# Kernel optimization log

Measured on AMD Instinct MI355X. Metric: run time of the kernel, lower is better.

Reference implementation:

```python
import jax, jax.numpy as jnp
import numpy as np

SOS = 4998
EOS = 4999
SCALING = 2.0


def setup_inputs() -> dict:
    key = jax.random.key(0)
    ks = jax.random.split(key, 12)
    B, T, E, D, A, C, F, ODIM, L = 32, 1000, 512, 1024, 512, 10, 100, 5000, 100
    s = 0.02
    return {
        "hpad": jax.random.normal(ks[0], (B, T, E), jnp.float32),
        "ys": jax.random.randint(ks[1], (B, L), 0, SOS, jnp.int32),
        # AttLoc params
        "w_enc": jax.random.normal(ks[2], (A, E), jnp.float32) * s,
        "b_enc": jnp.zeros((A,), jnp.float32),
        "w_dec": jax.random.normal(ks[3], (A, D), jnp.float32) * s,
        "w_att": jax.random.normal(ks[4], (A, C), jnp.float32) * s,
        "w_conv": jax.random.normal(ks[5], (C, 1, 2 * F + 1), jnp.float32) * s,  # OIH 1D conv kernel
        "w_gvec": jax.random.normal(ks[6], (1, A), jnp.float32) * s,
        "b_gvec": jnp.zeros((1,), jnp.float32),
        # Decoder params
        "embed": jax.random.normal(ks[7], (ODIM, D), jnp.float32) * s,
        "w_ih": jax.random.normal(ks[8], (4 * D, D + E), jnp.float32) * s,
        "w_hh": jax.random.normal(ks[9], (4 * D, D), jnp.float32) * s,
        "b_ih": jnp.zeros((4 * D,), jnp.float32),
        "b_hh": jnp.zeros((4 * D,), jnp.float32),
        "w_out": jax.random.normal(ks[10], (ODIM, D), jnp.float32) * s,
        "b_out": jnp.zeros((ODIM,), jnp.float32),
    }


def _decode(hpad, ys, w_enc, b_enc, w_dec, w_att, w_conv, w_gvec, b_gvec,
            embed, w_ih, w_hh, b_ih, b_hh, w_out, b_out):
    B, T, E = hpad.shape
    D = w_hh.shape[1]
    F = (w_conv.shape[-1] - 1) // 2
    # ys_in = [sos; y] per utterance (all same length -> already padded)
    ys_in = jnp.concatenate([jnp.full((B, 1), SOS, ys.dtype), ys], axis=1)  # [B, olen]
    eys = embed[ys_in]                                                      # [B, olen, D]
    # pre_compute_enc_h = mlp_enc(enc_h)
    pre = jnp.einsum('bte,ae->bta', hpad, w_enc) + b_enc                    # [B, T, A]
    att0 = jnp.full((B, T), 1.0 / T, hpad.dtype)   # uniform init attention (all hlen == T)
    z0 = jnp.zeros((B, D), hpad.dtype)
    c0 = jnp.zeros((B, D), hpad.dtype)

    def step(carry, ey_i):
        z, c, aw = carry
        # location-aware conv over previous attention weights: [B,1,T] -> [B,C,T]
        conv = jax.lax.conv_general_dilated(aw[:, None, :], w_conv, (1,), [(F, F)],
                                            dimension_numbers=('NCH', 'OIH', 'NCH'))
        att_feat = jnp.einsum('bct,ac->bta', conv, w_att)                   # mlp_att
        dec = (z @ w_dec.T)[:, None, :]                                     # mlp_dec, tiled
        e = jnp.tanh(att_feat + pre + dec) @ w_gvec[0] + b_gvec[0]          # [B, T]
        w = jax.nn.softmax(SCALING * e, axis=1)
        ctx = jnp.einsum('bt,bte->be', w, hpad)                             # [B, E]
        # LSTMCell
        x = jnp.concatenate([ey_i, ctx], axis=1)                            # [B, D+E]
        gates = x @ w_ih.T + b_ih + z @ w_hh.T + b_hh
        i_g, f_g, g_g, o_g = jnp.split(gates, 4, axis=1)
        c_new = jax.nn.sigmoid(f_g) * c + jax.nn.sigmoid(i_g) * jnp.tanh(g_g)
        z_new = jax.nn.sigmoid(o_g) * jnp.tanh(c_new)
        return (z_new, c_new, w), z_new

    _, z_all = jax.lax.scan(step, (z0, c0, att0), jnp.swapaxes(eys, 0, 1))  # [olen, B, D]
    y_all = jnp.einsum('obd,vd->obv', z_all, w_out) + b_out                 # [olen, B, odim]
    return jnp.swapaxes(y_all, 0, 1)                                        # [B, olen, odim]


def reference(hpad, ys, w_enc, b_enc, w_dec, w_att, w_conv, w_gvec, b_gvec,
              embed, w_ih, w_hh, b_ih, b_hh, w_out, b_out):
    return _decode(hpad, ys, w_enc, b_enc, w_dec, w_att, w_conv, w_gvec, b_gvec,
                   embed, w_ih, w_hh, b_ih, b_hh, w_out, b_out)
```

## Files before the change

kernel.cpp:

```cpp
#include <hip/hip_runtime.h>
#include <math.h>

#define B_    32
#define T_    1000
#define E_    512
#define D_    1024
#define A_    512
#define C_    10
#define F_    100
#define ODIM_ 5000
#define OLEN_ 101
#define SOS_  4998

#define OFF_PRE   0u
#define N_PRE     (32u*1000u*512u)
#define OFF_DEC   (OFF_PRE + N_PRE)
#define N_DEC     (32u*512u)
#define OFF_CONV  (OFF_DEC + N_DEC)
#define N_CONVB   (32u*10u*1000u)
#define OFF_SUM   OFF_CONV
#define OFF_EB    (OFF_CONV + N_CONVB)
#define N_EB      (32u*1000u)
#define OFF_AW    (OFF_EB + N_EB)
#define OFF_CTX   (OFF_AW + N_EB)
#define N_CTX     (32u*512u)
#define OFF_GP    (OFF_CTX + N_CTX)
#define N_GP      (10u*32u*4096u)
#define OFF_Z     (OFF_GP + N_GP)
#define N_Z       (32u*1024u)
#define OFF_C     (OFF_Z + N_Z)
#define OFF_ZALL  (OFF_C + N_Z)

__device__ __forceinline__ float fast_tanh(float x) {
    float cx = fminf(8.f, fmaxf(-8.f, x));
    float e = __expf(2.f * cx);
    return (e - 1.f) * __builtin_amdgcn_rcpf(e + 1.f);
}
__device__ __forceinline__ float fast_sigmoid(float x) {
    float cx = fminf(30.f, fmaxf(-30.f, x));
    return __builtin_amdgcn_rcpf(1.f + __expf(-cx));
}

__global__ __launch_bounds__(256) void k_init(float* ws) {
    int i = blockIdx.x * 256 + threadIdx.x;
    if (i < (int)N_Z) { ws[OFF_Z + i] = 0.f; ws[OFF_C + i] = 0.f; }
    if (i < (int)N_EB) ws[OFF_AW + i] = 1.0f / (float)T_;
    if (i < 32) ws[OFF_SUM + i] = 0.f;
}

__global__ __launch_bounds__(256) void k_pre(const float* __restrict__ hp,
                                             const float* __restrict__ we,
                                             const float* __restrict__ be,
                                             float* __restrict__ pre) {
    __shared__ float As[64][68];
    __shared__ float Bs[64][68];
    int m0 = blockIdx.y * 64, n0 = blockIdx.x * 64;
    int tid = threadIdx.x;
    int tr = tid >> 4, tc = tid & 15;
    float acc[4][4] = {};
    for (int k0 = 0; k0 < 512; k0 += 64) {
        for (int i = tid; i < 1024; i += 256) {
            int m = i >> 4, kq = (i & 15) << 2;
            float4 v = *(const float4*)&hp[(size_t)(m0 + m) * 512 + k0 + kq];
            As[kq + 0][m] = v.x; As[kq + 1][m] = v.y; As[kq + 2][m] = v.z; As[kq + 3][m] = v.w;
            float4 w = *(const float4*)&we[(size_t)(n0 + m) * 512 + k0 + kq];
            Bs[kq + 0][m] = w.x; Bs[kq + 1][m] = w.y; Bs[kq + 2][m] = w.z; Bs[kq + 3][m] = w.w;
        }
        __syncthreads();
        #pragma unroll 16
        for (int kk = 0; kk < 64; ++kk) {
            float4 av = *(const float4*)&As[kk][tr << 2];
            float4 bv = *(const float4*)&Bs[kk][tc << 2];
            float a[4] = {av.x, av.y, av.z, av.w};
            float b[4] = {bv.x, bv.y, bv.z, bv.w};
            #pragma unroll
            for (int i = 0; i < 4; i++)
                #pragma unroll
                for (int j = 0; j < 4; j++) acc[i][j] += a[i] * b[j];
        }
        __syncthreads();
    }
    #pragma unroll
    for (int i = 0; i < 4; i++) {
        int m = m0 + (tr << 2) + i;
        int n = n0 + (tc << 2);
        float4 o;
        o.x = acc[i][0] + be[n + 0];
        o.y = acc[i][1] + be[n + 1];
        o.z = acc[i][2] + be[n + 2];
        o.w = acc[i][3] + be[n + 3];
        *(float4*)&pre[(size_t)m * 512 + n] = o;
    }
}

__global__ __launch_bounds__(256) void k_dec(const float* __restrict__ wdec, float* ws) {
    int a = blockIdx.x * 4 + (threadIdx.x >> 6);
    int lane = threadIdx.x & 63;
    const float4* wr = (const float4*)(wdec + (size_t)a * 1024);
    float4 w4[4];
    #pragma unroll
    for (int j = 0; j < 4; j++) w4[j] = wr[j * 64 + lane];
    const float4* z4 = (const float4*)(ws + OFF_Z);
    for (int b = 0; b < 32; ++b) {
        float acc = 0.f;
        #pragma unroll
        for (int j = 0; j < 4; j++) {
            float4 z = z4[b * 256 + j * 64 + lane];
            acc += w4[j].x * z.x + w4[j].y * z.y + w4[j].z * z.z + w4[j].w * z.w;
        }
        #pragma unroll
        for (int off = 32; off > 0; off >>= 1) acc += __shfl_xor(acc, off, 64);
        if (lane == 0) ws[OFF_DEC + b * 512 + a] = acc;
    }
}

__global__ __launch_bounds__(512) void k_attn(const float* __restrict__ watt,
                                              const float* __restrict__ gvec,
                                              const float* __restrict__ bg,
                                              const float* __restrict__ wconv,
                                              float* ws) {
    __shared__ float aw_lds[328];
    __shared__ float conv_lds[10][126];
    __shared__ float psum;
    int b  = blockIdx.x >> 3;
    int tc = blockIdx.x & 7;
    int t0 = tc * 125;
    int tid = threadIdx.x;
    if (tid < 64) ws[OFF_CTX + b * 512 + tc * 64 + tid] = 0.f;
    if (tid == 0) psum = 0.f;
    if (tid < 328) {
        int tg = t0 - 100 + tid;
        aw_lds[tid] = (tg >= 0 && tg < 1000) ? ws[OFF_AW + b * 1000 + tg] : 0.f;
    }
    __syncthreads();
    for (int i = tid; i < 1250; i += 512) {
        int c = i / 125, tl = i - c * 125;
        const float* wc = wconv + c * 201;
        float acc = 0.f;
        #pragma unroll 4
        for (int j = 0; j < 201; ++j) acc += aw_lds[tl + j] * wc[j];
        conv_lds[c][tl] = acc;
    }
    int lane = tid & 63, w = tid >> 6;
    int a0 = lane * 4, a1 = 256 + lane * 4;
    float wr[8][10];
    #pragma unroll
    for (int i = 0; i < 4; i++)
        #pragma unroll
        for (int c = 0; c < 10; c++) {
            wr[i][c]     = watt[(a0 + i) * 10 + c];
            wr[4 + i][c] = watt[(a1 + i) * 10 + c];
        }
    float4 d0 = *(const float4*)&ws[OFF_DEC + b * 512 + a0];
    float4 d1 = *(const float4*)&ws[OFF_DEC + b * 512 + a1];
    float4 g0 = *(const float4*)&gvec[a0];
    float4 g1 = *(const float4*)&gvec[a1];
    float dc[8] = {d0.x, d0.y, d0.z, d0.w, d1.x, d1.y, d1.z, d1.w};
    float gv[8] = {g0.x, g0.y, g0.z, g0.w, g1.x, g1.y, g1.z, g1.w};
    float bgv = bg[0];
    __syncthreads();
    float lsum = 0.f;
    int tlo = w * 16, thi = tlo + 16; if (thi > 125) thi = 125;
    for (int tl = tlo; tl < thi; ++tl) {
        int t = t0 + tl;
        const float* pr = ws + OFF_PRE + (size_t)(b * 1000 + t) * 512;
        float4 p0 = *(const float4*)&pr[a0];
        float4 p1 = *(const float4*)&pr[a1];
        float cv[10];
        #pragma unroll
        for (int c = 0; c < 10; c++) cv[c] = conv_lds[c][tl];
        float pa[8] = {p0.x, p0.y, p0.z, p0.w, p1.x, p1.y, p1.z, p1.w};
        float acc = 0.f;
        #pragma unroll
        for (int i = 0; i < 8; i++) {
            float s = pa[i] + dc[i];
            #pragma unroll
            for (int c = 0; c < 10; c++) s += cv[c] * wr[i][c];
            acc += gv[i] * fast_tanh(s);
        }
        #pragma unroll
        for (int off = 32; off > 0; off >>= 1) acc += __shfl_xor(acc, off, 64);
        if (lane == 0) {
            float p = __expf(2.f * (acc + bgv));
            ws[OFF_EB + b * 1000 + t] = p;
            lsum += p;
        }
    }
    if (lane == 0) atomicAdd(&psum, lsum);
    __syncthreads();
    if (tid == 0) atomicAdd(&ws[OFF_SUM + b], psum);
}

__global__ __launch_bounds__(128) void k_ctx(const float* __restrict__ hp, float* ws) {
    int b = blockIdx.x >> 5, ts = blockIdx.x & 31;
    int t0 = ts * 32;
    int t1 = t0 + 32; if (t1 > 1000) t1 = 1000;
    int tid = threadIdx.x;
    float inv = __builtin_amdgcn_rcpf(ws[OFF_SUM + b]);
    const float* pb = ws + OFF_EB + b * 1000;
    if (tid < t1 - t0) ws[OFF_AW + b * 1000 + t0 + tid] = pb[t0 + tid] * inv;
    const float4* hp4 = (const float4*)hp;
    float4 acc = make_float4(0.f, 0.f, 0.f, 0.f);
    for (int t = t0; t < t1; ++t) {
        float w = pb[t] * inv;
        float4 h = hp4[(size_t)(b * 1000 + t) * 128 + tid];
        acc.x += w * h.x; acc.y += w * h.y; acc.z += w * h.z; acc.w += w * h.w;
    }
    float* cx = ws + OFF_CTX + b * 512 + tid * 4;
    atomicAdd(cx + 0, acc.x); atomicAdd(cx + 1, acc.y);
    atomicAdd(cx + 2, acc.z); atomicAdd(cx + 3, acc.w);
}

__global__ __launch_bounds__(128) void k_gates(const float* __restrict__ wih,
                                               const float* __restrict__ whh,
                                               const float* __restrict__ embed,
                                               const int* __restrict__ ys,
                                               float* ws, int step) {
    __shared__ float wlds[32][68];
    __shared__ float xs[32][36];
    int nt = blockIdx.x & 63;
    int ks = blockIdx.x >> 6;
    int n0 = nt * 64;
    int tid = threadIdx.x;
    int nq = tid & 15, bq = tid >> 4;
    float acc[4][4] = {};
    for (int kc = 0; kc < 8; ++kc) {
        int k0 = ks * 256 + kc * 32;
        {
            int r = tid >> 1, h = tid & 1;
            int gn = n0 + r;
            const float* wrow = (k0 < 1536)
                ? (wih + (size_t)gn * 1536 + k0 + h * 16)
                : (whh + (size_t)gn * 1024 + (k0 - 1536) + h * 16);
            #pragma unroll
            for (int j = 0; j < 4; ++j) {
                float4 v = *(const float4*)&wrow[j * 4];
                int kb = h * 16 + j * 4;
                wlds[kb + 0][r] = v.x; wlds[kb + 1][r] = v.y;
                wlds[kb + 2][r] = v.z; wlds[kb + 3][r] = v.w;
            }
        }
        {
            int b = tid >> 2, q = tid & 3;
            int tok = (step == 0) ? SOS_ : ys[b * 100 + step - 1];
            #pragma unroll
            for (int j = 0; j < 2; ++j) {
                int kk = k0 + q * 8 + j * 4;
                float4 v;
                if (kk < 1024)       v = *(const float4*)&embed[(size_t)tok * 1024 + kk];
                else if (kk < 1536)  v = *(const float4*)&ws[OFF_CTX + b * 512 + kk - 1024];
                else                 v = *(const float4*)&ws[OFF_Z + b * 1024 + kk - 1536];
                int kb = q * 8 + j * 4;
                xs[kb + 0][b] = v.x; xs[kb + 1][b] = v.y;
                xs[kb + 2][b] = v.z; xs[kb + 3][b] = v.w;
            }
        }
        __syncthreads();
        #pragma unroll 8
        for (int kk = 0; kk < 32; ++kk) {
            float4 wv = *(const float4*)&wlds[kk][nq * 4];
            float4 xv = *(const float4*)&xs[kk][bq * 4];
            float wa[4] = {wv.x, wv.y, wv.z, wv.w};
            float xa[4] = {xv.x, xv.y, xv.z, xv.w};
            #pragma unroll
            for (int i = 0; i < 4; i++)
                #pragma unroll
                for (int j = 0; j < 4; j++) acc[i][j] += wa[i] * xa[j];
        }
        __syncthreads();
    }
    float* gp = ws + OFF_GP + (size_t)(ks * 32 + bq * 4) * 4096 + n0 + nq * 4;
    #pragma unroll
    for (int j = 0; j < 4; j++)
        #pragma unroll
        for (int i = 0; i < 4; i++)
            gp[(size_t)j * 4096 + i] = acc[i][j];
}

__global__ __launch_bounds__(256) void k_lstm(const float* __restrict__ bih,
                                              const float* __restrict__ bhh,
                                              float* ws, int step) {
    if (blockIdx.x == 0 && threadIdx.x < 32) ws[OFF_SUM + threadIdx.x] = 0.f;
    int id = blockIdx.x * 256 + threadIdx.x;
    int b = id >> 10, d = id & 1023;
    float gi = bih[d] + bhh[d];
    float gf = bih[1024 + d] + bhh[1024 + d];
    float gg = bih[2048 + d] + bhh[2048 + d];
    float go = bih[3072 + d] + bhh[3072 + d];
    const float* gp = ws + OFF_GP;
    #pragma unroll
    for (int kc = 0; kc < 10; kc++) {
        const float* r = gp + (size_t)(kc * 32 + b) * 4096;
        gi += r[d];
        gf += r[1024 + d];
        gg += r[2048 + d];
        go += r[3072 + d];
    }
    float c_old = ws[OFF_C + id];
    float si = fast_sigmoid(gi);
    float sf = fast_sigmoid(gf);
    float so = fast_sigmoid(go);
    float cn = sf * c_old + si * fast_tanh(gg);
    float h = so * fast_tanh(cn);
    ws[OFF_C + id] = cn;
    ws[OFF_Z + id] = h;
    ws[OFF_ZALL + ((size_t)step * 32 + b) * 1024 + d] = h;
}

__global__ __launch_bounds__(256) void k_out(const float* __restrict__ zall,
                                             const float* __restrict__ wo,
                                             const float* __restrict__ bo,
                                             float* __restrict__ out) {
    __shared__ float As[64][68];
    __shared__ float Bs[64][68];
    int m0 = blockIdx.y * 64, n0 = blockIdx.x * 64;
    int tid = threadIdx.x;
    int tr = tid >> 4, tc = tid & 15;
    float acc[4][4] = {};
    for (int k0 = 0; k0 < 1024; k0 += 64) {
        for (int i = tid; i < 1024; i += 256) {
            int m = i >> 4, kq = (i & 15) << 2;
            int gm = m0 + m;
            float4 v = (gm < 3232) ? *(const float4*)&zall[(size_t)gm * 1024 + k0 + kq]
                                   : make_float4(0.f, 0.f, 0.f, 0.f);
            As[kq + 0][m] = v.x; As[kq + 1][m] = v.y; As[kq + 2][m] = v.z; As[kq + 3][m] = v.w;
            int gn = n0 + m;
            float4 w = (gn < 5000) ? *(const float4*)&wo[(size_t)gn * 1024 + k0 + kq]
                                   : make_float4(0.f, 0.f, 0.f, 0.f);
            Bs[kq + 0][m] = w.x; Bs[kq + 1][m] = w.y; Bs[kq + 2][m] = w.z; Bs[kq + 3][m] = w.w;
        }
        __syncthreads();
        #pragma unroll 16
        for (int kk = 0; kk < 64; ++kk) {
            float4 av = *(const float4*)&As[kk][tr << 2];
            float4 bv = *(const float4*)&Bs[kk][tc << 2];
            float a[4] = {av.x, av.y, av.z, av.w};
            float b[4] = {bv.x, bv.y, bv.z, bv.w};
            #pragma unroll
            for (int i = 0; i < 4; i++)
                #pragma unroll
                for (int j = 0; j < 4; j++) acc[i][j] += a[i] * b[j];
        }
        __syncthreads();
    }
    #pragma unroll
    for (int i = 0; i < 4; i++) {
        int m = m0 + (tr << 2) + i;
        if (m >= 3232) continue;
        int b = m & 31, o = m >> 5;
        #pragma unroll
        for (int j = 0; j < 4; j++) {
            int v = n0 + (tc << 2) + j;
            if (v < 5000)
                out[((size_t)b * 101 + o) * 5000 + v] = acc[i][j] + bo[v];
        }
    }
}

extern "C" void kernel_launch(void* const* d_in, const int* in_sizes, int n_in,
                              void* d_out, int out_size, void* d_ws, size_t ws_size,
                              hipStream_t stream) {
    const float* hpad   = (const float*)d_in[0];
    const int*   ys     = (const int*)d_in[1];
    const float* w_enc  = (const float*)d_in[2];
    const float* b_enc  = (const float*)d_in[3];
    const float* w_dec  = (const float*)d_in[4];
    const float* w_att  = (const float*)d_in[5];
    const float* w_conv = (const float*)d_in[6];
    const float* w_gvec = (const float*)d_in[7];
    const float* b_gvec = (const float*)d_in[8];
    const float* embed  = (const float*)d_in[9];
    const float* w_ih   = (const float*)d_in[10];
    const float* w_hh   = (const float*)d_in[11];
    const float* b_ih   = (const float*)d_in[12];
    const float* b_hh   = (const float*)d_in[13];
    const float* w_out  = (const float*)d_in[14];
    const float* b_out  = (const float*)d_in[15];
    float* ws  = (float*)d_ws;
    float* out = (float*)d_out;

    k_init<<<128, 256, 0, stream>>>(ws);
    k_pre<<<dim3(8, 500), 256, 0, stream>>>(hpad, w_enc, b_enc, ws + OFF_PRE);

    for (int step = 0; step < OLEN_; ++step) {
        k_dec<<<128, 256, 0, stream>>>(w_dec, ws);
        k_attn<<<256, 512, 0, stream>>>(w_att, w_gvec, b_gvec, w_conv, ws);
        k_ctx<<<1024, 128, 0, stream>>>(hpad, ws);
        k_gates<<<640, 128, 0, stream>>>(w_ih, w_hh, embed, ys, ws, step);
        k_lstm<<<128, 256, 0, stream>>>(b_ih, b_hh, ws, step);
    }

    k_out<<<dim3(79, 51), 256, 0, stream>>>(ws + OFF_ZALL, w_out, b_out, out);
}
```

Before: 12.43 ms.

## Split attention into parallel prep (dec+conv) and energy kernels with deferred normalization

Folds the decoder projection, the location convolution (now a standalone, globally parallel pass over unnormalized energies, scaled by the reciprocal of the previous sum) and the context/sum zeroing into a single k_prep launch. A separate k_energy kernel computes the tanh/gvec energies with more blocks and a coalesced layout for the transposed w_att. Softmax sums use double-buffered slots, so k_ctx no longer writes normalized attention back and k_lstm no longer clears the sums. The goal is more parallelism and less redundant per-block convolution work. The cost is an extra workspace round-trip for the conv output and more atomics on the sums.

```diff
diff --git a/kernel.cpp b/kernel.cpp
--- a/kernel.cpp
+++ b/kernel.cpp
@@ -18,10 +18,11 @@
 #define N_DEC     (32u*512u)
 #define OFF_CONV  (OFF_DEC + N_DEC)
 #define N_CONVB   (32u*10u*1000u)
-#define OFF_SUM   OFF_CONV
 #define OFF_EB    (OFF_CONV + N_CONVB)
 #define N_EB      (32u*1000u)
 #define OFF_AW    (OFF_EB + N_EB)
+#define OFF_SW    OFF_AW
+#define OFF_WATT  (OFF_AW + 64u)
 #define OFF_CTX   (OFF_AW + N_EB)
 #define N_CTX     (32u*512u)
 #define OFF_GP    (OFF_CTX + N_CTX)
@@ -41,11 +42,13 @@
     return __builtin_amdgcn_rcpf(1.f + __expf(-cx));
 }
 
-__global__ __launch_bounds__(256) void k_init(float* ws) {
+__global__ __launch_bounds__(256) void k_init(const float* __restrict__ watt, float* ws) {
     int i = blockIdx.x * 256 + threadIdx.x;
     if (i < (int)N_Z) { ws[OFF_Z + i] = 0.f; ws[OFF_C + i] = 0.f; }
-    if (i < (int)N_EB) ws[OFF_AW + i] = 1.0f / (float)T_;
-    if (i < 32) ws[OFF_SUM + i] = 0.f;
+    if (i < (int)N_EB) ws[OFF_EB + i] = 1.0f / (float)T_;
+    if (i < 32) ws[OFF_SW + i] = 1.0f;
+    else if (i < 64) ws[OFF_SW + i] = 0.f;
+    if (i < 5120) ws[OFF_WATT + i] = watt[(i & 511) * 10 + (i >> 9)];
 }
 
 __global__ __launch_bounds__(256) void k_pre(const float* __restrict__ hp,
@@ -93,112 +96,116 @@
     }
 }
 
-__global__ __launch_bounds__(256) void k_dec(const float* __restrict__ wdec, float* ws) {
-    int a = blockIdx.x * 4 + (threadIdx.x >> 6);
-    int lane = threadIdx.x & 63;
-    const float4* wr = (const float4*)(wdec + (size_t)a * 1024);
-    float4 w4[4];
+__global__ __launch_bounds__(256) void k_prep(const float* __restrict__ wdec,
+                                              const float* __restrict__ wconv,
+                                              float* ws, int rslot, int wslot) {
+    int tid = threadIdx.x;
+    if (blockIdx.x < 512) {
+        int wid = blockIdx.x * 4 + (tid >> 6);
+        int a = wid >> 2, bq = wid & 3;
+        int lane = tid & 63;
+        const float4* wr = (const float4*)(wdec + (size_t)a * 1024);
+        float4 w4[4];
+        #pragma unroll
+        for (int j = 0; j < 4; j++) w4[j] = wr[j * 64 + lane];
+        const float4* z4 = (const float4*)(ws + OFF_Z);
+        #pragma unroll
+        for (int i = 0; i < 8; ++i) {
+            int b = bq * 8 + i;
+            float acc = 0.f;
+            #pragma unroll
+            for (int j = 0; j < 4; j++) {
+                float4 z = z4[b * 256 + j * 64 + lane];
+                acc += w4[j].x * z.x + w4[j].y * z.y + w4[j].z * z.z + w4[j].w * z.w;
+            }
+            #pragma unroll
+            for (int off = 32; off > 0; off >>= 1) acc += __shfl_xor(acc, off, 64);
+            if (lane == 0) ws[OFF_DEC + b * 512 + a] = acc;
+        }
+    } else if (blockIdx.x < 832) {
+        int blk = blockIdx.x - 512;
+        int b = blk / 10, c = blk - b * 10;
+        if (tid >= 250) return;
+        int t = tid * 4;
+        float inv = __builtin_amdgcn_rcpf(ws[OFF_SW + rslot * 32 + b]);
+        const float* ar = ws + OFF_EB + b * 1000;
+        const float* wc = wconv + c * 201;
+        float a0, a1, a2, a3;
+        a0 = (t - 100 >= 0) ? ar[t - 100] : 0.f;
+        a1 = (t -  99 >= 0) ? ar[t -  99] : 0.f;
+        a2 = (t -  98 >= 0) ? ar[t -  98] : 0.f;
+        a3 = (t -  97 >= 0) ? ar[t -  97] : 0.f;
+        float c0 = 0.f, c1 = 0.f, c2 = 0.f, c3 = 0.f;
+        #pragma unroll 4
+        for (int j = 0; j < 201; ++j) {
+            float w = wc[j];
+            c0 += a0 * w; c1 += a1 * w; c2 += a2 * w; c3 += a3 * w;
+            a0 = a1; a1 = a2; a2 = a3;
+            int ni = t + j - 96;
+            a3 = (ni >= 0 && ni < 1000) ? ar[ni] : 0.f;
+        }
+        float* o = ws + OFF_CONV + (size_t)(b * 10 + c) * 1000 + t;
+        o[0] = c0 * inv; o[1] = c1 * inv; o[2] = c2 * inv; o[3] = c3 * inv;
+    } else if (blockIdx.x == 832) {
+        if (tid < 32) ws[OFF_SW + wslot * 32 + tid] = 0.f;
+    } else {
+        int idx = (blockIdx.x - 833) * 1024 + tid * 4;
+        *(float4*)&ws[OFF_CTX + idx] = make_float4(0.f, 0.f, 0.f, 0.f);
+    }
+}
+
+__global__ __launch_bounds__(256) void k_energy(const float* __restrict__ gvec,
+                                                const float* __restrict__ bg,
+                                                float* ws, int wslot) {
+    int b  = blockIdx.x >> 4;
+    int t0 = (blockIdx.x & 15) * 63;
+    int t1 = t0 + 63; if (t1 > 1000) t1 = 1000;
+    int lane = threadIdx.x & 63, w = threadIdx.x >> 6;
+    const float* wattT = ws + OFF_WATT;
+    float wr[8][10], dc[8], gv[8];
     #pragma unroll
-    for (int j = 0; j < 4; j++) w4[j] = wr[j * 64 + lane];
-    const float4* z4 = (const float4*)(ws + OFF_Z);
-    for (int b = 0; b < 32; ++b) {
+    for (int i = 0; i < 8; i++) {
+        int a = i * 64 + lane;
+        #pragma unroll
+        for (int c = 0; c < 10; c++) wr[i][c] = wattT[c * 512 + a];
+        dc[i] = ws[OFF_DEC + b * 512 + a];
+        gv[i] = gvec[a];
+    }
+    float bgv = bg[0];
+    const float* convb = ws + OFF_CONV + (size_t)b * 10000;
+    float lsum = 0.f;
+    for (int t = t0 + w; t < t1; t += 4) {
+        const float* pr = ws + OFF_PRE + (size_t)(b * 1000 + t) * 512;
+        float cv[10];
+        #pragma unroll
+        for (int c = 0; c < 10; c++) cv[c] = convb[c * 1000 + t];
         float acc = 0.f;
         #pragma unroll
-        for (int j = 0; j < 4; j++) {
-            float4 z = z4[b * 256 + j * 64 + lane];
-            acc += w4[j].x * z.x + w4[j].y * z.y + w4[j].z * z.z + w4[j].w * z.w;
-        }
-        #pragma unroll
-        for (int off = 32; off > 0; off >>= 1) acc += __shfl_xor(acc, off, 64);
-        if (lane == 0) ws[OFF_DEC + b * 512 + a] = acc;
-    }
-}
-
-__global__ __launch_bounds__(512) void k_attn(const float* __restrict__ watt,
-                                              const float* __restrict__ gvec,
-                                              const float* __restrict__ bg,
-                                              const float* __restrict__ wconv,
-                                              float* ws) {
-    __shared__ float aw_lds[328];
-    __shared__ float conv_lds[10][126];
-    __shared__ float psum;
-    int b  = blockIdx.x >> 3;
-    int tc = blockIdx.x & 7;
-    int t0 = tc * 125;
-    int tid = threadIdx.x;
-    if (tid < 64) ws[OFF_CTX + b * 512 + tc * 64 + tid] = 0.f;
-    if (tid == 0) psum = 0.f;
-    if (tid < 328) {
-        int tg = t0 - 100 + tid;
-        aw_lds[tid] = (tg >= 0 && tg < 1000) ? ws[OFF_AW + b * 1000 + tg] : 0.f;
-    }
-    __syncthreads();
-    for (int i = tid; i < 1250; i += 512) {
-        int c = i / 125, tl = i - c * 125;
-        const float* wc = wconv + c * 201;
-        float acc = 0.f;
-        #pragma unroll 4
-        for (int j = 0; j < 201; ++j) acc += aw_lds[tl + j] * wc[j];
-        conv_lds[c][tl] = acc;
-    }
-    int lane = tid & 63, w = tid >> 6;
-    int a0 = lane * 4, a1 = 256 + lane * 4;
-    float wr[8][10];
-    #pragma unroll
-    for (int i = 0; i < 4; i++)
-        #pragma unroll
-        for (int c = 0; c < 10; c++) {
-            wr[i][c]     = watt[(a0 + i) * 10 + c];
-            wr[4 + i][c] = watt[(a1 + i) * 10 + c];
-        }
-    float4 d0 = *(const float4*)&ws[OFF_DEC + b * 512 + a0];
-    float4 d1 = *(const float4*)&ws[OFF_DEC + b * 512 + a1];
-    float4 g0 = *(const float4*)&gvec[a0];
-    float4 g1 = *(const float4*)&gvec[a1];
-    float dc[8] = {d0.x, d0.y, d0.z, d0.w, d1.x, d1.y, d1.z, d1.w};
-    float gv[8] = {g0.x, g0.y, g0.z, g0.w, g1.x, g1.y, g1.z, g1.w};
-    float bgv = bg[0];
-    __syncthreads();
-    float lsum = 0.f;
-    int tlo = w * 16, thi = tlo + 16; if (thi > 125) thi = 125;
-    for (int tl = tlo; tl < thi; ++tl) {
-        int t = t0 + tl;
-        const float* pr = ws + OFF_PRE + (size_t)(b * 1000 + t) * 512;
-        float4 p0 = *(const float4*)&pr[a0];
-        float4 p1 = *(const float4*)&pr[a1];
-        float cv[10];
-        #pragma unroll
-        for (int c = 0; c < 10; c++) cv[c] = conv_lds[c][tl];
-        float pa[8] = {p0.x, p0.y, p0.z, p0.w, p1.x, p1.y, p1.z, p1.w};
-        float acc = 0.f;
-        #pragma unroll
         for (int i = 0; i < 8; i++) {
-            float s = pa[i] + dc[i];
+            float s = pr[i * 64 + lane] + dc[i];
             #pragma unroll
             for (int c = 0; c < 10; c++) s += cv[c] * wr[i][c];
             acc += gv[i] * fast_tanh(s);
         }
         #pragma unroll
         for (int off = 32; off > 0; off >>= 1) acc += __shfl_xor(acc, off, 64);
+        float p = __expf(2.f * (acc + bgv));
         if (lane == 0) {
-            float p = __expf(2.f * (acc + bgv));
             ws[OFF_EB + b * 1000 + t] = p;
             lsum += p;
         }
     }
-    if (lane == 0) atomicAdd(&psum, lsum);
-    __syncthreads();
-    if (tid == 0) atomicAdd(&ws[OFF_SUM + b], psum);
-}
-
-__global__ __launch_bounds__(128) void k_ctx(const float* __restrict__ hp, float* ws) {
+    if (lane == 0) atomicAdd(&ws[OFF_SW + wslot * 32 + b], lsum);
+}
+
+__global__ __launch_bounds__(128) void k_ctx(const float* __restrict__ hp,
+                                             float* ws, int wslot) {
     int b = blockIdx.x >> 5, ts = blockIdx.x & 31;
     int t0 = ts * 32;
     int t1 = t0 + 32; if (t1 > 1000) t1 = 1000;
     int tid = threadIdx.x;
-    float inv = __builtin_amdgcn_rcpf(ws[OFF_SUM + b]);
+    float inv = __builtin_amdgcn_rcpf(ws[OFF_SW + wslot * 32 + b]);
     const float* pb = ws + OFF_EB + b * 1000;
-    if (tid < t1 - t0) ws[OFF_AW + b * 1000 + t0 + tid] = pb[t0 + tid] * inv;
     const float4* hp4 = (const float4*)hp;
     float4 acc = make_float4(0.f, 0.f, 0.f, 0.f);
     for (int t = t0; t < t1; ++t) {
@@ -280,7 +287,6 @@
 __global__ __launch_bounds__(256) void k_lstm(const float* __restrict__ bih,
                                               const float* __restrict__ bhh,
                                               float* ws, int step) {
-    if (blockIdx.x == 0 && threadIdx.x < 32) ws[OFF_SUM + threadIdx.x] = 0.f;
     int id = blockIdx.x * 256 + threadIdx.x;
     int b = id >> 10, d = id & 1023;
     float gi = bih[d] + bhh[d];
@@ -379,13 +385,14 @@
     float* ws  = (float*)d_ws;
     float* out = (float*)d_out;
 
-    k_init<<<128, 256, 0, stream>>>(ws);
+    k_init<<<128, 256, 0, stream>>>(w_att, ws);
     k_pre<<<dim3(8, 500), 256, 0, stream>>>(hpad, w_enc, b_enc, ws + OFF_PRE);
 
     for (int step = 0; step < OLEN_; ++step) {
-        k_dec<<<128, 256, 0, stream>>>(w_dec, ws);
-        k_attn<<<256, 512, 0, stream>>>(w_att, w_gvec, b_gvec, w_conv, ws);
-        k_ctx<<<1024, 128, 0, stream>>>(hpad, ws);
+        int rslot = step & 1, wslot = (step + 1) & 1;
+        k_prep<<<849, 256, 0, stream>>>(w_dec, w_conv, ws, rslot, wslot);
+        k_energy<<<512, 256, 0, stream>>>(w_gvec, b_gvec, ws, wslot);
+        k_ctx<<<1024, 128, 0, stream>>>(hpad, ws, wslot);
         k_gates<<<640, 128, 0, stream>>>(w_ih, w_hh, embed, ys, ws, step);
         k_lstm<<<128, 256, 0, stream>>>(b_ih, b_hh, ws, step);
     }
```

New measurement: 14.31 ms. +15.1%, slower.
